# Performance work log

Hardware: AMD Instinct MI355X
Metric: run time of the kernel (lower is better)

The kernel has to match this reference:

```python
import jax, jax.numpy as jnp
import numpy as np

TOP_K = 8
ROUTED_SCALING_FACTOR = 1.5


def setup_inputs() -> dict:
    key = jax.random.key(0)
    k1, k2, k3 = jax.random.split(key, 3)
    T, D, E = 16384, 4096, 256  # tokens, hidden_size, n_routed_experts
    hidden_states = jax.random.normal(k1, (T, D), dtype=jnp.float32)
    W = jax.random.normal(k2, (E, D), dtype=jnp.float32) * (1.0 / np.sqrt(D))
    e_score_correction_bias = jax.random.normal(k3, (E,), dtype=jnp.float32) * 0.1
    return {"hidden_states": hidden_states, "W": W,
            "e_score_correction_bias": e_score_correction_bias}


def reference(hidden_states, W, e_score_correction_bias):
    # classifier: dense router GEMM [T, D] x [D, E] -> [T, E]
    classify_score = jnp.einsum('td,ed->te', hidden_states, W)
    # routing: softmax -> bias-corrected top-k selection -> gather of
    # UNbiased softmax scores, scaled.
    scores = jax.nn.softmax(classify_score, axis=-1)            # [T, E]
    scores_for_choice = scores + e_score_correction_bias[None]  # [T, E]
    _, topk_indices = jax.lax.top_k(scores_for_choice, TOP_K)   # [T, k]
    topk_weights = jnp.take_along_axis(scores, topk_indices, axis=-1)
    topk_weights = topk_weights.astype(jnp.float32) * ROUTED_SCALING_FACTOR
    return classify_score, topk_weights, topk_indices.astype(jnp.int32)
```

## Files before the change

### kernel.cpp

```cpp
#include <hip/hip_runtime.h>
#include <hip/hip_bf16.h>
#include <cstdint>


typedef __attribute__((ext_vector_type(8))) short short8;
typedef __attribute__((ext_vector_type(16))) float f32x16;

#define T_TOK  16384
#define DIM    4096
#define NE     256
#define TOPK_N 8

__device__ __forceinline__ float bf2f_u(unsigned short h) {
  return __uint_as_float(((unsigned int)h) << 16);
}
__device__ __forceinline__ unsigned cvt_pk2(float f0, float f1) {
  __hip_bfloat162 h2 = __float22bfloat162_rn(float2{f0, f1});
  unsigned u;
  __builtin_memcpy(&u, &h2, 4);
  return u;
}
__device__ __forceinline__ void split8(const float* f, uint4& hv, uint4& lv) {
  unsigned h[4], l[4];
#pragma unroll
  for (int c = 0; c < 4; ++c) {
    float a = f[2 * c], b = f[2 * c + 1];
    h[c] = cvt_pk2(a, b);
    float ra = a - bf2f_u((unsigned short)(h[c] & 0xffffu));
    float rb = b - bf2f_u((unsigned short)(h[c] >> 16));
    l[c] = cvt_pk2(ra, rb);
  }
  hv = uint4{h[0], h[1], h[2], h[3]};
  lv = uint4{l[0], l[1], l[2], l[3]};
}

__global__ __launch_bounds__(256) void convert_w_kernel(
    const float* __restrict__ W,
    unsigned short* __restrict__ Whp,
    unsigned short* __restrict__ Wlp) {
  const int t = blockIdx.x * 256 + threadIdx.x;
  const int e = t >> 9, k8 = t & 511;
  const int nt = e >> 5, col = e & 31;
  const int s = k8 >> 1, h = k8 & 1;
  const float* src = W + (size_t)e * DIM + k8 * 8;
  float f[8];
  *(float4*)(f)     = *(const float4*)src;
  *(float4*)(f + 4) = *(const float4*)(src + 4);
  uint4 hv, lv;
  split8(f, hv, lv);
  const size_t dst = ((size_t)(nt * 256 + s) * 64 + h * 32 + col) * 8;
  *(uint4*)(Whp + dst) = hv;
  *(uint4*)(Wlp + dst) = lv;
}

__device__ __forceinline__ f32x16 mfma32(short8 a, short8 b, f32x16 c) {
  return __builtin_amdgcn_mfma_f32_32x32x16_bf16(a, b, c, 0, 0, 0);
}

template <bool ATOMIC>
__global__ __launch_bounds__(256, 2) void gemm_router(
    const float* __restrict__ A,
    const unsigned short* __restrict__ Whp,
    const unsigned short* __restrict__ Wlp,
    float* C0,
    float* C1) {
  __shared__ __align__(16) unsigned short Ash[2][2][2][8][64][8];

  const int tid  = threadIdx.x;
  const int w    = tid >> 6, l = tid & 63;
  const int band = blockIdx.x & 255;
  const int kh   = blockIdx.x >> 8;
  const size_t kbase = (size_t)kh * 2048;
  float* C = (ATOMIC || kh == 0) ? C0 : C1;

  const int srow = tid >> 2, kg = tid & 3;
  const int smt = srow >> 5, sr = srow & 31;
  const float* ap = A + (size_t)(band * 64 + srow) * DIM + kbase + kg * 32;

  const unsigned short* ph0 = Whp + ((size_t)(2 * w)     * 256 + kh * 128) * 512 + (size_t)l * 8;
  const unsigned short* pl0 = Wlp + ((size_t)(2 * w)     * 256 + kh * 128) * 512 + (size_t)l * 8;
  const unsigned short* ph1 = Whp + ((size_t)(2 * w + 1) * 256 + kh * 128) * 512 + (size_t)l * 8;
  const unsigned short* pl1 = Wlp + ((size_t)(2 * w + 1) * 256 + kh * 128) * 512 + (size_t)l * 8;

  f32x16 acc00 = {}, acc01 = {}, acc10 = {}, acc11 = {};
  float ar[32];

#pragma unroll
  for (int i = 0; i < 8; ++i)
    *(float4*)(ar + i * 4) = *(const float4*)(ap + i * 4);
  {
#pragma unroll
    for (int sub = 0; sub < 2; ++sub) {
      uint4 hv0, lv0, hv1, lv1;
      split8(ar + sub * 16,     hv0, lv0);
      split8(ar + sub * 16 + 8, hv1, lv1);
      const int ks = kg * 2 + sub;
      *(uint4*)&Ash[0][0][smt][ks][ 0 + sr][0] = hv0;
      *(uint4*)&Ash[0][0][smt][ks][32 + sr][0] = hv1;
      *(uint4*)&Ash[0][1][smt][ks][ 0 + sr][0] = lv0;
      *(uint4*)&Ash[0][1][smt][ks][32 + sr][0] = lv1;
    }
  }
#pragma unroll
  for (int i = 0; i < 8; ++i)
    *(float4*)(ar + i * 4) = *(const float4*)(ap + 128 + i * 4);

  short8 b[2][4];
  b[0][0] = *(const short8*)(ph0);
  b[0][1] = *(const short8*)(pl0);
  b[0][2] = *(const short8*)(ph1);
  b[0][3] = *(const short8*)(pl1);
  b[1][0] = *(const short8*)(ph0 + 512);
  b[1][1] = *(const short8*)(pl0 + 512);
  b[1][2] = *(const short8*)(ph1 + 512);
  b[1][3] = *(const short8*)(pl1 + 512);

  for (int c = 0; c < 16; ++c) {
    const int buf = c & 1;
    asm volatile("s_waitcnt lgkmcnt(0)" ::: "memory");
    __builtin_amdgcn_s_barrier();
    asm volatile("" ::: "memory");

#pragma unroll
    for (int ks = 0; ks < 8; ++ks) {
      const int gs = c * 8 + ks;
      short8 B0h = b[gs & 1][0], B0l = b[gs & 1][1];
      short8 B1h = b[gs & 1][2], B1l = b[gs & 1][3];
      const size_t gp = (size_t)((gs + 2 < 128) ? gs + 2 : gs) * 512;
      b[gs & 1][0] = *(const short8*)(ph0 + gp);
      b[gs & 1][1] = *(const short8*)(pl0 + gp);
      b[gs & 1][2] = *(const short8*)(ph1 + gp);
      b[gs & 1][3] = *(const short8*)(pl1 + gp);

      short8 a0h = *(const short8*)&Ash[buf][0][0][ks][l][0];
      short8 a0l = *(const short8*)&Ash[buf][1][0][ks][l][0];
      short8 a1h = *(const short8*)&Ash[buf][0][1][ks][l][0];
      short8 a1l = *(const short8*)&Ash[buf][1][1][ks][l][0];

      __builtin_amdgcn_s_setprio(1);
      acc00 = mfma32(a0h, B0h, acc00);  acc01 = mfma32(a0h, B1h, acc01);
      acc10 = mfma32(a1h, B0h, acc10);  acc11 = mfma32(a1h, B1h, acc11);
      acc00 = mfma32(a0l, B0h, acc00);  acc01 = mfma32(a0l, B1h, acc01);
      acc10 = mfma32(a1l, B0h, acc10);  acc11 = mfma32(a1l, B1h, acc11);
      acc00 = mfma32(a0h, B0l, acc00);  acc01 = mfma32(a0h, B1l, acc01);
      acc10 = mfma32(a1h, B0l, acc10);  acc11 = mfma32(a1h, B1l, acc11);
      __builtin_amdgcn_s_setprio(0);
    }

    if (c < 15) {
#pragma unroll
      for (int sub = 0; sub < 2; ++sub) {
        uint4 hv0, lv0, hv1, lv1;
        split8(ar + sub * 16,     hv0, lv0);
        split8(ar + sub * 16 + 8, hv1, lv1);
        const int ks = kg * 2 + sub;
        *(uint4*)&Ash[buf ^ 1][0][smt][ks][ 0 + sr][0] = hv0;
        *(uint4*)&Ash[buf ^ 1][0][smt][ks][32 + sr][0] = hv1;
        *(uint4*)&Ash[buf ^ 1][1][smt][ks][ 0 + sr][0] = lv0;
        *(uint4*)&Ash[buf ^ 1][1][smt][ks][32 + sr][0] = lv1;
      }
      if (c + 2 < 16) {
#pragma unroll
        for (int i = 0; i < 8; ++i)
          *(float4*)(ar + i * 4) = *(const float4*)(ap + (size_t)(c + 2) * 128 + i * 4);
      }
    }
  }

  const int rb = band * 64 + 4 * (l >> 5);
  const int cb = w * 64 + (l & 31);
#pragma unroll
  for (int r = 0; r < 16; ++r) {
    const int row = rb + (r & 3) + 8 * (r >> 2);
    if (ATOMIC) {
      unsafeAtomicAdd(&C[(size_t)row * NE + cb],             acc00[r]);
      unsafeAtomicAdd(&C[(size_t)row * NE + cb + 32],        acc01[r]);
      unsafeAtomicAdd(&C[(size_t)(row + 32) * NE + cb],      acc10[r]);
      unsafeAtomicAdd(&C[(size_t)(row + 32) * NE + cb + 32], acc11[r]);
    } else {
      C[(size_t)row * NE + cb]             = acc00[r];
      C[(size_t)row * NE + cb + 32]        = acc01[r];
      C[(size_t)(row + 32) * NE + cb]      = acc10[r];
      C[(size_t)(row + 32) * NE + cb + 32] = acc11[r];
    }
  }
}

template <bool FUSE>
__global__ __launch_bounds__(256) void topk_kernel(
    const float* __restrict__ Cp0, const float* __restrict__ Cp1,
    const float* __restrict__ bias, float* __restrict__ classify,
    float* __restrict__ wOut, float* __restrict__ iOut) {
  const int wave = threadIdx.x >> 6;
  const int lane = threadIdx.x & 63;
  const int tok  = blockIdx.x * 4 + wave;

  float4 c4 = *(const float4*)(Cp0 + (size_t)tok * NE + lane * 4);
  if (FUSE) {
    float4 p4 = *(const float4*)(Cp1 + (size_t)tok * NE + lane * 4);
    c4.x += p4.x; c4.y += p4.y; c4.z += p4.z; c4.w += p4.w;
    *(float4*)(classify + (size_t)tok * NE + lane * 4) = c4;
  }
  float v[4] = {c4.x, c4.y, c4.z, c4.w};

  float mx = fmaxf(fmaxf(v[0], v[1]), fmaxf(v[2], v[3]));
#pragma unroll
  for (int off = 32; off >= 1; off >>= 1) mx = fmaxf(mx, __shfl_xor(mx, off));

  float e0 = __expf(v[0] - mx), e1 = __expf(v[1] - mx);
  float e2 = __expf(v[2] - mx), e3 = __expf(v[3] - mx);
  float sum = e0 + e1 + e2 + e3;
#pragma unroll
  for (int off = 32; off >= 1; off >>= 1) sum += __shfl_xor(sum, off);

  float sc0 = e0 / sum, sc1 = e1 / sum, sc2 = e2 / sum, sc3 = e3 / sum;
  float4 b4 = *(const float4*)(bias + lane * 4);
  float ch0 = sc0 + b4.x, ch1 = sc1 + b4.y, ch2 = sc2 + b4.z, ch3 = sc3 + b4.w;

#pragma unroll
  for (int t = 0; t < TOPK_N; ++t) {
    float bv = ch0; int bi = 0; float bs = sc0;
    if (ch1 > bv) { bv = ch1; bi = 1; bs = sc1; }
    if (ch2 > bv) { bv = ch2; bi = 2; bs = sc2; }
    if (ch3 > bv) { bv = ch3; bi = 3; bs = sc3; }
    int be = lane * 4 + bi;
#pragma unroll
    for (int off = 32; off >= 1; off >>= 1) {
      float ov = __shfl_xor(bv, off);
      int   oe = __shfl_xor(be, off);
      float os = __shfl_xor(bs, off);
      if (ov > bv || (ov == bv && oe < be)) { bv = ov; be = oe; bs = os; }
    }
    if (lane == 0) {
      wOut[tok * TOPK_N + t] = bs * 1.5f;
      iOut[tok * TOPK_N + t] = (float)be;
    }
    bool own = (be >> 2) == lane;
    int  lb  = be & 3;
    if (own && lb == 0) ch0 = -INFINITY;
    if (own && lb == 1) ch1 = -INFINITY;
    if (own && lb == 2) ch2 = -INFINITY;
    if (own && lb == 3) ch3 = -INFINITY;
  }
}

extern "C" void kernel_launch(void* const* d_in, const int* in_sizes, int n_in,
                              void* d_out, int out_size, void* d_ws, size_t ws_size,
                              hipStream_t stream) {
  const float* hs   = (const float*)d_in[0];
  const float* W    = (const float*)d_in[1];
  const float* bias = (const float*)d_in[2];

  float* out      = (float*)d_out;
  float* classify = out;
  float* wOut     = out + (size_t)T_TOK * NE;
  float* iOut     = wOut + (size_t)T_TOK * TOPK_N;

  unsigned short* Whp = (unsigned short*)d_ws;
  unsigned short* Wlp = Whp + (size_t)NE * DIM;

  const size_t wpack_bytes = (size_t)NE * DIM * 2 * sizeof(unsigned short);
  const size_t part_bytes  = (size_t)T_TOK * NE * sizeof(float);
  float* p1 = (float*)((char*)d_ws + wpack_bytes);

  convert_w_kernel<<<(NE * DIM / 8) / 256, 256, 0, stream>>>(W, Whp, Wlp);

  if (ws_size >= wpack_bytes + part_bytes) {
    gemm_router<false><<<512, 256, 0, stream>>>(hs, Whp, Wlp, classify, p1);
    topk_kernel<true><<<T_TOK / 4, 256, 0, stream>>>(classify, p1, bias,
                                                     classify, wOut, iOut);
  } else {
    hipMemsetAsync(classify, 0, part_bytes, stream);
    gemm_router<true><<<512, 256, 0, stream>>>(hs, Whp, Wlp, classify, classify);
    topk_kernel<false><<<T_TOK / 4, 256, 0, stream>>>(classify, nullptr, bias,
                                                      classify, wOut, iOut);
  }
}
```

Baseline: 428.5 us.

## Split router GEMM tile across 8 waves with one expert tile each

```diff
diff --git a/kernel.cpp b/kernel.cpp
--- a/kernel.cpp
+++ b/kernel.cpp
@@ -58,7 +58,7 @@
 }
 
 template <bool ATOMIC>
-__global__ __launch_bounds__(256, 2) void gemm_router(
+__global__ __launch_bounds__(512, 4) void gemm_router(
     const float* __restrict__ A,
     const unsigned short* __restrict__ Whp,
     const unsigned short* __restrict__ Wlp,
@@ -73,47 +73,37 @@
   const size_t kbase = (size_t)kh * 2048;
   float* C = (ATOMIC || kh == 0) ? C0 : C1;
 
-  const int srow = tid >> 2, kg = tid & 3;
+  const int srow = tid >> 3, kg = tid & 7;
   const int smt = srow >> 5, sr = srow & 31;
-  const float* ap = A + (size_t)(band * 64 + srow) * DIM + kbase + kg * 32;
-
-  const unsigned short* ph0 = Whp + ((size_t)(2 * w)     * 256 + kh * 128) * 512 + (size_t)l * 8;
-  const unsigned short* pl0 = Wlp + ((size_t)(2 * w)     * 256 + kh * 128) * 512 + (size_t)l * 8;
-  const unsigned short* ph1 = Whp + ((size_t)(2 * w + 1) * 256 + kh * 128) * 512 + (size_t)l * 8;
-  const unsigned short* pl1 = Wlp + ((size_t)(2 * w + 1) * 256 + kh * 128) * 512 + (size_t)l * 8;
-
-  f32x16 acc00 = {}, acc01 = {}, acc10 = {}, acc11 = {};
-  float ar[32];
-
-#pragma unroll
-  for (int i = 0; i < 8; ++i)
+  const float* ap = A + (size_t)(band * 64 + srow) * DIM + kbase + kg * 16;
+
+  const unsigned short* ph = Whp + ((size_t)w * 256 + kh * 128) * 512 + (size_t)l * 8;
+  const unsigned short* pl = Wlp + ((size_t)w * 256 + kh * 128) * 512 + (size_t)l * 8;
+
+  f32x16 acc0 = {}, acc1 = {};
+  float ar[16];
+
+#pragma unroll
+  for (int i = 0; i < 4; ++i)
     *(float4*)(ar + i * 4) = *(const float4*)(ap + i * 4);
   {
-#pragma unroll
-    for (int sub = 0; sub < 2; ++sub) {
-      uint4 hv0, lv0, hv1, lv1;
-      split8(ar + sub * 16,     hv0, lv0);
-      split8(ar + sub * 16 + 8, hv1, lv1);
-      const int ks = kg * 2 + sub;
-      *(uint4*)&Ash[0][0][smt][ks][ 0 + sr][0] = hv0;
-      *(uint4*)&Ash[0][0][smt][ks][32 + sr][0] = hv1;
-      *(uint4*)&Ash[0][1][smt][ks][ 0 + sr][0] = lv0;
-      *(uint4*)&Ash[0][1][smt][ks][32 + sr][0] = lv1;
-    }
-  }
-#pragma unroll
-  for (int i = 0; i < 8; ++i)
+    uint4 hv0, lv0, hv1, lv1;
+    split8(ar,     hv0, lv0);
+    split8(ar + 8, hv1, lv1);
+    *(uint4*)&Ash[0][0][smt][kg][ 0 + sr][0] = hv0;
+    *(uint4*)&Ash[0][0][smt][kg][32 + sr][0] = hv1;
+    *(uint4*)&Ash[0][1][smt][kg][ 0 + sr][0] = lv0;
+    *(uint4*)&Ash[0][1][smt][kg][32 + sr][0] = lv1;
+  }
+#pragma unroll
+  for (int i = 0; i < 4; ++i)
     *(float4*)(ar + i * 4) = *(const float4*)(ap + 128 + i * 4);
 
-  short8 b[2][4];
-  b[0][0] = *(const short8*)(ph0);
-  b[0][1] = *(const short8*)(pl0);
-  b[0][2] = *(const short8*)(ph1);
-  b[0][3] = *(const short8*)(pl1);
-  b[1][0] = *(const short8*)(ph0 + 512);
-  b[1][1] = *(const short8*)(pl0 + 512);
-  b[1][2] = *(const short8*)(ph1 + 512);
-  b[1][3] = *(const short8*)(pl1 + 512);
+  short8 b[2][2];
+  b[0][0] = *(const short8*)(ph);
+  b[0][1] = *(const short8*)(pl);
+  b[1][0] = *(const short8*)(ph + 512);
+  b[1][1] = *(const short8*)(pl + 512);
 
   for (int c = 0; c < 16; ++c) {
     const int buf = c & 1;
@@ -124,13 +114,10 @@
 #pragma unroll
     for (int ks = 0; ks < 8; ++ks) {
       const int gs = c * 8 + ks;
-      short8 B0h = b[gs & 1][0], B0l = b[gs & 1][1];
-      short8 B1h = b[gs & 1][2], B1l = b[gs & 1][3];
+      short8 Bh = b[gs & 1][0], Bl = b[gs & 1][1];
       const size_t gp = (size_t)((gs + 2 < 128) ? gs + 2 : gs) * 512;
-      b[gs & 1][0] = *(const short8*)(ph0 + gp);
-      b[gs & 1][1] = *(const short8*)(pl0 + gp);
-      b[gs & 1][2] = *(const short8*)(ph1 + gp);
-      b[gs & 1][3] = *(const short8*)(pl1 + gp);
+      b[gs & 1][0] = *(const short8*)(ph + gp);
+      b[gs & 1][1] = *(const short8*)(pl + gp);
 
       short8 a0h = *(const short8*)&Ash[buf][0][0][ks][l][0];
       short8 a0l = *(const short8*)&Ash[buf][1][0][ks][l][0];
@@ -138,50 +125,41 @@
       short8 a1l = *(const short8*)&Ash[buf][1][1][ks][l][0];
 
       __builtin_amdgcn_s_setprio(1);
-      acc00 = mfma32(a0h, B0h, acc00);  acc01 = mfma32(a0h, B1h, acc01);
-      acc10 = mfma32(a1h, B0h, acc10);  acc11 = mfma32(a1h, B1h, acc11);
-      acc00 = mfma32(a0l, B0h, acc00);  acc01 = mfma32(a0l, B1h, acc01);
-      acc10 = mfma32(a1l, B0h, acc10);  acc11 = mfma32(a1l, B1h, acc11);
-      acc00 = mfma32(a0h, B0l, acc00);  acc01 = mfma32(a0h, B1l, acc01);
-      acc10 = mfma32(a1h, B0l, acc10);  acc11 = mfma32(a1h, B1l, acc11);
+      acc0 = mfma32(a0h, Bh, acc0);  acc1 = mfma32(a1h, Bh, acc1);
+      acc0 = mfma32(a0l, Bh, acc0);  acc1 = mfma32(a1l, Bh, acc1);
+      acc0 = mfma32(a0h, Bl, acc0);  acc1 = mfma32(a1h, Bl, acc1);
       __builtin_amdgcn_s_setprio(0);
     }
 
     if (c < 15) {
-#pragma unroll
-      for (int sub = 0; sub < 2; ++sub) {
+      {
         uint4 hv0, lv0, hv1, lv1;
-        split8(ar + sub * 16,     hv0, lv0);
-        split8(ar + sub * 16 + 8, hv1, lv1);
-        const int ks = kg * 2 + sub;
-        *(uint4*)&Ash[buf ^ 1][0][smt][ks][ 0 + sr][0] = hv0;
-        *(uint4*)&Ash[buf ^ 1][0][smt][ks][32 + sr][0] = hv1;
-        *(uint4*)&Ash[buf ^ 1][1][smt][ks][ 0 + sr][0] = lv0;
-        *(uint4*)&Ash[buf ^ 1][1][smt][ks][32 + sr][0] = lv1;
+        split8(ar,     hv0, lv0);
+        split8(ar + 8, hv1, lv1);
+        *(uint4*)&Ash[buf ^ 1][0][smt][kg][ 0 + sr][0] = hv0;
+        *(uint4*)&Ash[buf ^ 1][0][smt][kg][32 + sr][0] = hv1;
+        *(uint4*)&Ash[buf ^ 1][1][smt][kg][ 0 + sr][0] = lv0;
+        *(uint4*)&Ash[buf ^ 1][1][smt][kg][32 + sr][0] = lv1;
       }
       if (c + 2 < 16) {
 #pragma unroll
-        for (int i = 0; i < 8; ++i)
+        for (int i = 0; i < 4; ++i)
           *(float4*)(ar + i * 4) = *(const float4*)(ap + (size_t)(c + 2) * 128 + i * 4);
       }
     }
   }
 
   const int rb = band * 64 + 4 * (l >> 5);
-  const int cb = w * 64 + (l & 31);
+  const int cb = w * 32 + (l & 31);
 #pragma unroll
   for (int r = 0; r < 16; ++r) {
     const int row = rb + (r & 3) + 8 * (r >> 2);
     if (ATOMIC) {
-      unsafeAtomicAdd(&C[(size_t)row * NE + cb],             acc00[r]);
-      unsafeAtomicAdd(&C[(size_t)row * NE + cb + 32],        acc01[r]);
-      unsafeAtomicAdd(&C[(size_t)(row + 32) * NE + cb],      acc10[r]);
-      unsafeAtomicAdd(&C[(size_t)(row + 32) * NE + cb + 32], acc11[r]);
+      unsafeAtomicAdd(&C[(size_t)row * NE + cb],        acc0[r]);
+      unsafeAtomicAdd(&C[(size_t)(row + 32) * NE + cb], acc1[r]);
     } else {
-      C[(size_t)row * NE + cb]             = acc00[r];
-      C[(size_t)row * NE + cb + 32]        = acc01[r];
-      C[(size_t)(row + 32) * NE + cb]      = acc10[r];
-      C[(size_t)(row + 32) * NE + cb + 32] = acc11[r];
+      C[(size_t)row * NE + cb]        = acc0[r];
+      C[(size_t)(row + 32) * NE + cb] = acc1[r];
     }
   }
 }
@@ -266,12 +244,12 @@
   convert_w_kernel<<<(NE * DIM / 8) / 256, 256, 0, stream>>>(W, Whp, Wlp);
 
   if (ws_size >= wpack_bytes + part_bytes) {
-    gemm_router<false><<<512, 256, 0, stream>>>(hs, Whp, Wlp, classify, p1);
+    gemm_router<false><<<512, 512, 0, stream>>>(hs, Whp, Wlp, classify, p1);
     topk_kernel<true><<<T_TOK / 4, 256, 0, stream>>>(classify, p1, bias,
                                                      classify, wOut, iOut);
   } else {
     hipMemsetAsync(classify, 0, part_bytes, stream);
-    gemm_router<true><<<512, 256, 0, stream>>>(hs, Whp, Wlp, classify, classify);
+    gemm_router<true><<<512, 512, 0, stream>>>(hs, Whp, Wlp, classify, classify);
     topk_kernel<false><<<T_TOK / 4, 256, 0, stream>>>(classify, nullptr, bias,
                                                       classify, wOut, iOut);
   }
```

New measurement: 426.1 us. About the same (-0.6%).
